# Kernel tuning notes

Hardware: AMD Instinct MI355X
Metric: run time of the kernel (lower is better)

Reference implementation:

```python
import jax, jax.numpy as jnp
import numpy as np
from jax.scipy.special import gammainc

ALPH = 0.8  # significance level (default arg in original forward)


def _median_width(X, iu, ju):
    # pairwise squared distances; original takes median of strictly-positive
    # strict-upper-triangle entries (tril subtracted) -> median over triu(k=1)
    G = jnp.sum(X * X, axis=1)                    # [n]
    D = G[:, None] + G[None, :] - 2.0 * (X @ X.T)  # [n, n]
    du = D[iu, ju]                                 # strict upper triangle, static size
    return jnp.sqrt(0.5 * jnp.median(du))


def _rbf(X, width):
    G = jnp.sum(X * X, axis=1)
    D = G[:, None] + G[None, :] - 2.0 * (X @ X.T)
    return jnp.exp(-D / (2.0 * width ** 2))


def _center(K):
    # H K H with H = I - 11^T/n  ==  K - rowmean - colmean + totalmean
    cm = jnp.mean(K, axis=0, keepdims=True)   # mean over rows  -> [1, n]
    rm = jnp.mean(K, axis=1, keepdims=True)   # mean over cols  -> [n, 1]
    tm = jnp.mean(K)
    return K - cm - rm + tm


def _gamma_ppf(a, p):
    # invert regularized lower incomplete gamma via fixed-iteration bisection
    hi0 = a + 10.0 * jnp.sqrt(a) + 100.0
    def body(i, lohi):
        lo, hi = lohi
        mid = 0.5 * (lo + hi)
        below = gammainc(a, mid) < p
        return (jnp.where(below, mid, lo), jnp.where(below, hi, mid))
    lo, hi = jax.lax.fori_loop(0, 100, body, (jnp.zeros_like(a), hi0))
    return 0.5 * (lo + hi)


def setup_inputs() -> dict:
    key = jax.random.key(0)
    k1, k2 = jax.random.split(key)
    X = jax.random.normal(k1, (4096, 64), dtype=jnp.float32)
    Y = jax.random.normal(k2, (4096, 64), dtype=jnp.float32)
    return {"X": X, "Y": Y}


def reference(X, Y):
    n = X.shape[0]
    iu, ju = np.triu_indices(n, k=1)  # static index set

    width_x = _median_width(X, iu, ju)
    width_y = _median_width(Y, iu, ju)

    K = _rbf(X, width_x)
    L = _rbf(Y, width_y)

    Kc = _center(K)
    Lc = _center(L)

    testStat = jnp.sum(Kc.T * Lc) / n

    V = (Kc * Lc / 6.0) ** 2
    varHSIC = (jnp.sum(V) - jnp.trace(V)) / n / (n - 1)
    varHSIC = varHSIC * 72.0 * (n - 4) * (n - 5) / n / (n - 1) / (n - 2) / (n - 3)

    # zero-diagonal kernels for mean estimate
    K0sum = jnp.sum(K) - jnp.trace(K)
    L0sum = jnp.sum(L) - jnp.trace(L)
    muX = K0sum / n / (n - 1)
    muY = L0sum / n / (n - 1)
    mHSIC = (1.0 + muX * muY - muX - muY) / n

    al = mHSIC ** 2 / varHSIC
    bet = varHSIC * n / mHSIC
    thresh = bet * _gamma_ppf(al, jnp.float32(1.0 - ALPH))
    return (testStat, thresh)
```

## Files before the change

kernel.cpp:

```cpp
#include <hip/hip_runtime.h>

typedef unsigned int u32;
typedef unsigned short u16;
typedef __attribute__((ext_vector_type(8))) short bf16x8;
typedef __attribute__((ext_vector_type(4))) float f32x4;

#define NPTS 4096
#define DIM  64
#define NB   32
#define NBLK 528
#define WLO16 0x4140u
#define NWBIN 832
#define RSTR 836
#define KF1C 8390654u
#define KF2C 8390656u


__device__ __forceinline__ void bmap(int b, int& by, int& bx){
  by = 0;
  while (b >= NB - by){ b -= NB - by; by++; }
  bx = by + b;
}

__device__ __forceinline__ u16 f2bf(float x){
  u32 u = __float_as_uint(x);
  return (u16)((u + 0x7fffu + ((u>>16)&1u)) >> 16);
}

__global__ __launch_bounds__(256) void convert_k(const float* __restrict__ X, const float* __restrict__ Y,
                                                 u16* __restrict__ Xbf, float* __restrict__ Gall,
                                                 u32* __restrict__ histsum, double* __restrict__ rowK,
                                                 double* __restrict__ rowL, double* __restrict__ sumsS,
                                                 double* __restrict__ slotbuf, u32* __restrict__ ctr){
  int t = blockIdx.x*256 + threadIdx.x;
  int rid = t >> 1, hf = t & 1;
  int z = rid >> 12, row = rid & 4095;
  const float* src = (z ? Y : X) + (size_t)row*DIM + hf*32;
  u16* basep = Xbf + ((size_t)z*32768 + (size_t)(row>>4)*128 + (row&15))*8;
  float g = 0.f;
#pragma unroll
  for (int f=0; f<4; f++){
    float4 f0 = *(const float4*)(src + f*8);
    float4 f1 = *(const float4*)(src + f*8 + 4);
    g = fmaf(f0.x,f0.x,g); g = fmaf(f0.y,f0.y,g); g = fmaf(f0.z,f0.z,g); g = fmaf(f0.w,f0.w,g);
    g = fmaf(f1.x,f1.x,g); g = fmaf(f1.y,f1.y,g); g = fmaf(f1.z,f1.z,g); g = fmaf(f1.w,f1.w,g);
    ushort4 h0, h1;
    h0.x=f2bf(f0.x); h0.y=f2bf(f0.y); h0.z=f2bf(f0.z); h0.w=f2bf(f0.w);
    h1.x=f2bf(f1.x); h1.y=f2bf(f1.y); h1.z=f2bf(f1.z); h1.w=f2bf(f1.w);
    u16* dst = basep + (size_t)(hf*4 + f)*16*8;
    *(ushort4*)dst = h0;
    *(ushort4*)(dst+4) = h1;
  }
  g += __shfl_xor(g, 1, 64);
  if (hf==0) Gall[rid] = g;
  if (t < NPTS){ rowK[t] = 0.0; rowL[t] = 0.0; }
  if (t < 2*RSTR) histsum[t] = 0u;
  if (t < 64) slotbuf[t] = 0.0;
  if (t < 16) sumsS[t] = 0.0;
  if (t == 0) *ctr = 0u;
}

__global__ __launch_bounds__(256,2) void hist_k(const u16* __restrict__ Xbf, const float* __restrict__ Gall,
                                                u32* __restrict__ histsum){
  __shared__ u32 lh[4][RSTR];
  int z = blockIdx.y, tid = threadIdx.x;
  int by,bx; bmap(blockIdx.x, by, bx);
  bool isdiag = (by==bx);
  u32 wgt = isdiag ? 1u : 2u;
  int w=tid>>6, lane=tid&63, q=lane>>4, nl=lane&15;
  int cp = lane & 3;
  for (int t=tid;t<4*RSTR;t+=256) ((u32*)lh)[t]=0;
  __syncthreads();
  const bf16x8* Xb = (const bf16x8*)Xbf + (size_t)z*32768;
  const float* Gz = Gall + z*NPTS;
  int ag0 = by*8 + w, ag1 = by*8 + 4 + w;
  bf16x8 a0f0 = Xb[ag0*128 + q*16 + nl];
  bf16x8 a0f1 = Xb[ag0*128 + (4+q)*16 + nl];
  bf16x8 a1f0 = Xb[ag1*128 + q*16 + nl];
  bf16x8 a1f1 = Xb[ag1*128 + (4+q)*16 + nl];
  float ga0 = Gz[ag0*16 + nl], ga1 = Gz[ag1*16 + nl];
  float g0m[4], g1m[4];
#pragma unroll
  for (int r=0;r<4;r++){ g0m[r] = __shfl(ga0, q*4+r, 64); g1m[r] = __shfl(ga1, q*4+r, 64); }
#pragma unroll
  for (int tb=0;tb<8;tb++){
    int jg = bx*8 + tb;
    bf16x8 bf0 = Xb[jg*128 + q*16 + nl];
    bf16x8 bf1 = Xb[jg*128 + (4+q)*16 + nl];
    f32x4 acc0 = (f32x4)0.0f, acc1 = (f32x4)0.0f;
    acc0 = __builtin_amdgcn_mfma_f32_16x16x32_bf16(a0f0, bf0, acc0, 0,0,0);
    acc0 = __builtin_amdgcn_mfma_f32_16x16x32_bf16(a0f1, bf1, acc0, 0,0,0);
    acc1 = __builtin_amdgcn_mfma_f32_16x16x32_bf16(a1f0, bf0, acc1, 0,0,0);
    acc1 = __builtin_amdgcn_mfma_f32_16x16x32_bf16(a1f1, bf1, acc1, 0,0,0);
    int j = jg*16 + nl;
    float gb = Gz[j];
#pragma unroll
    for (int r=0;r<4;r++){
      float d0 = (g0m[r] + gb) - 2.0f*acc0[r];
      float d1 = (g1m[r] + gb) - 2.0f*acc1[r];
      if (isdiag){
        if (ag0*16 + q*4 + r == j) d0 = 0.f;
        if (ag1*16 + q*4 + r == j) d1 = 0.f;
      }
      u32 t0 = __float_as_uint(d0) >> 16;
      u32 bin0 = (t0 < WLO16) ? 0u : (t0 >= WLO16+NWBIN) ? (u32)(NWBIN+1) : (t0 - WLO16 + 1u);
      atomicAdd(&lh[cp][bin0], wgt);
      u32 t1 = __float_as_uint(d1) >> 16;
      u32 bin1 = (t1 < WLO16) ? 0u : (t1 >= WLO16+NWBIN) ? (u32)(NWBIN+1) : (t1 - WLO16 + 1u);
      atomicAdd(&lh[cp][bin1], wgt);
    }
  }
  __syncthreads();
  u32* dst = histsum + (size_t)z*RSTR;
  for (int t=tid;t<RSTR;t+=256){
    u32 v = lh[0][t] + lh[1][t] + lh[2][t] + lh[3][t];
    if (v) atomicAdd(&dst[t], v);
  }
}

__global__ __launch_bounds__(256,2) void rowsum_k(const u16* __restrict__ Xbf, const float* __restrict__ Gall,
                                                  const u32* __restrict__ histsum, float* __restrict__ scal,
                                                  double* __restrict__ rowK, double* __restrict__ rowL,
                                                  double* __restrict__ sumsS){
  __shared__ union {
    struct { u32 wsum[4]; double svals[2]; float scal_sh; } sc;
    struct { double rowacc[128]; double colLDS[4][128]; double tred[2]; } rs;
  } sh;
  int z = blockIdx.y, tid = threadIdx.x;
  int w=tid>>6, lane=tid&63, q=lane>>4, nl=lane&15;

  {
    u32 c4[4] = {0,0,0,0};
    if (tid < 209){
      const u32* base = histsum + (size_t)z*RSTR + 4*tid;
      int lim = RSTR - 4*tid;
      c4[0] = base[0];
      if (lim>1) c4[1] = base[1];
      if (lim>2) c4[2] = base[2];
      if (lim>3) c4[3] = base[3];
    }
    u32 s = c4[0]+c4[1]+c4[2]+c4[3];
    u32 pre = s;
#pragma unroll
    for (int off=1; off<64; off<<=1){
      u32 t2 = __shfl_up(pre, off, 64);
      if (lane >= off) pre += t2;
    }
    if (lane==63) sh.sc.wsum[w] = pre;
    __syncthreads();
    u32 base2 = 0;
    for (int k=0;k<w;k++) base2 += sh.sc.wsum[k];
    u32 incl = base2 + pre, excl = incl - s;
    u32 ks[2] = {KF1C,KF2C};
#pragma unroll
    for (int w2=0; w2<2; w2++){
      if (ks[w2] >= excl && ks[w2] < incl){
        u32 acc = excl;
#pragma unroll
        for (int j=0;j<4;j++){
          if (ks[w2] < acc + c4[j]){
            int b = tid*4 + j;
            double lo, hi;
            if (b==0){ lo=12.0; hi=12.0; }
            else if (b>=NWBIN+1){ lo=1024.0; hi=1024.0; }
            else {
              u32 t16 = WLO16 + (u32)b - 1u;
              lo = (double)__uint_as_float(t16<<16);
              hi = (double)__uint_as_float((t16+1u)<<16);
            }
            double frac = ((double)(ks[w2]-acc) + 0.5)/(double)c4[j];
            sh.sc.svals[w2] = lo + (hi-lo)*frac;
            break;
          }
          acc += c4[j];
        }
      }
    }
    __syncthreads();
    if (tid==0){
      float med = (float)(0.5*(sh.sc.svals[0]+sh.sc.svals[1]));
      float wd = sqrtf(0.5f*med);
      float sc2 = 2.0f*wd*wd;
      sh.sc.scal_sh = sc2;
      if (blockIdx.x==0) scal[z] = sc2;
    }
    __syncthreads();
  }
  float negi = -1.0f / sh.sc.scal_sh;
  __syncthreads();

  int by,bx; bmap(blockIdx.x, by, bx);
  bool isdiag = (by==bx);
  const bf16x8* Xb = (const bf16x8*)Xbf + (size_t)z*32768;
  const float* Gz = Gall + z*NPTS;
  int ag0 = by*8 + w, ag1 = by*8 + 4 + w;
  bf16x8 a0f0 = Xb[ag0*128 + q*16 + nl];
  bf16x8 a0f1 = Xb[ag0*128 + (4+q)*16 + nl];
  bf16x8 a1f0 = Xb[ag1*128 + q*16 + nl];
  bf16x8 a1f1 = Xb[ag1*128 + (4+q)*16 + nl];
  float ga0 = Gz[ag0*16 + nl], ga1 = Gz[ag1*16 + nl];
  float g0m[4], g1m[4];
#pragma unroll
  for (int r=0;r<4;r++){ g0m[r] = __shfl(ga0, q*4+r, 64); g1m[r] = __shfl(ga1, q*4+r, 64); }
  double rs0[4] = {0,0,0,0}, rs1[4] = {0,0,0,0};
#pragma unroll
  for (int tb=0;tb<8;tb++){
    int jg = bx*8 + tb;
    bf16x8 bf0 = Xb[jg*128 + q*16 + nl];
    bf16x8 bf1 = Xb[jg*128 + (4+q)*16 + nl];
    f32x4 acc0 = (f32x4)0.0f, acc1 = (f32x4)0.0f;
    acc0 = __builtin_amdgcn_mfma_f32_16x16x32_bf16(a0f0, bf0, acc0, 0,0,0);
    acc0 = __builtin_amdgcn_mfma_f32_16x16x32_bf16(a0f1, bf1, acc0, 0,0,0);
    acc1 = __builtin_amdgcn_mfma_f32_16x16x32_bf16(a1f0, bf0, acc1, 0,0,0);
    acc1 = __builtin_amdgcn_mfma_f32_16x16x32_bf16(a1f1, bf1, acc1, 0,0,0);
    int j = jg*16 + nl;
    float gb = Gz[j];
    double cs = 0.0;
#pragma unroll
    for (int r=0;r<4;r++){
      float d0 = (g0m[r] + gb) - 2.0f*acc0[r];
      float d1 = (g1m[r] + gb) - 2.0f*acc1[r];
      if (isdiag){
        if (ag0*16 + q*4 + r == j) d0 = 0.f;
        if (ag1*16 + q*4 + r == j) d1 = 0.f;
      }
      double e0 = (double)expf(d0*negi);
      double e1 = (double)expf(d1*negi);
      rs0[r] += e0; rs1[r] += e1;
      cs += e0 + e1;
    }
    cs += __shfl_xor(cs, 16, 64);
    cs += __shfl_xor(cs, 32, 64);
    if (q==0) sh.rs.colLDS[w][tb*16 + nl] = cs;
  }
#pragma unroll
  for (int r=0;r<4;r++){
    double v0 = rs0[r], v1 = rs1[r];
    v0 += __shfl_xor(v0,1,64); v0 += __shfl_xor(v0,2,64);
    v0 += __shfl_xor(v0,4,64); v0 += __shfl_xor(v0,8,64);
    v1 += __shfl_xor(v1,1,64); v1 += __shfl_xor(v1,2,64);
    v1 += __shfl_xor(v1,4,64); v1 += __shfl_xor(v1,8,64);
    rs0[r] = v0; rs1[r] = v1;
  }
  if (nl==0){
#pragma unroll
    for (int r=0;r<4;r++){
      sh.rs.rowacc[w*16 + q*4 + r]     = rs0[r];
      sh.rs.rowacc[(4+w)*16 + q*4 + r] = rs1[r];
    }
  }
  __syncthreads();
  double tot = 0.0;
  if (tid < 128){
    double rv = sh.rs.rowacc[tid];
    double cv = sh.rs.colLDS[0][tid] + sh.rs.colLDS[1][tid] + sh.rs.colLDS[2][tid] + sh.rs.colLDS[3][tid];
    double* rowG = z ? rowL : rowK;
    atomicAdd(&rowG[by*128 + tid], rv);
    if (!isdiag) atomicAdd(&rowG[bx*128 + tid], cv);
    tot = rv + (isdiag ? 0.0 : cv);
  }
#pragma unroll
  for (int s2=1;s2<64;s2<<=1) tot += __shfl_xor(tot, s2, 64);
  if (lane==0 && w<2) sh.rs.tred[w] = tot;
  __syncthreads();
  if (tid==0) atomicAdd(&sumsS[z*8 + (blockIdx.x & 7)], sh.rs.tred[0] + sh.rs.tred[1]);
}

__device__ double gammainc_wave(double a, double x, double lga, int lane){
  double C = 1.0/a;
  double psum = 0.0;
  for (int b=0;b<8192;b++){
    double k = (double)(b*64 + lane + 1);
    double rr = x/(a+k);
    double pp = rr;
#pragma unroll
    for (int s=1;s<64;s<<=1){
      double t = __shfl_up(pp, s, 64);
      if (lane >= s) pp *= t;
    }
    double c = C*pp;
    psum += c;
    double clast = __shfl(c, 63, 64);
    double rlast = __shfl(rr, 63, 64);
    C = clast;
    if (rlast < 1.0 && clast*rlast/(1.0-rlast) < 1e-17) break;
  }
#pragma unroll
  for (int s=1;s<64;s<<=1) psum += __shfl_xor(psum, s, 64);
  double total = 1.0/a + psum;
  return exp(-x + a*log(x) - lga) * total;
}

__global__ __launch_bounds__(256,2) void final_k(const u16* __restrict__ Xbf, const float* __restrict__ Gall,
                                                 const float* __restrict__ scal,
                                                 const double* __restrict__ rowK,
                                                 const double* __restrict__ rowL,
                                                 const double* __restrict__ sumsS,
                                                 double* __restrict__ slotbuf, u32* __restrict__ ctr,
                                                 float* __restrict__ out){
  __shared__ double red[4][3];
  __shared__ int lastFlag;
  int tid = threadIdx.x;
  int b = blockIdx.x >> 1, half = blockIdx.x & 1;
  int by,bx; bmap(b,by,bx);
  bool isdiag = (by==bx);
  int w=tid>>6, lane=tid&63, q=lane>>4, nl=lane&15;
  const bf16x8* Xb = (const bf16x8*)Xbf;
  const bf16x8* Yb = Xb + 32768;
  const float* Gx = Gall;
  const float* Gy = Gall + NPTS;
  const double inv_n = 1.0/(double)NPTS;
  double sK=0.0, sL=0.0;
#pragma unroll
  for (int k2=0;k2<8;k2++){ sK += sumsS[k2]; sL += sumsS[8+k2]; }
  double tmK = sK*(inv_n*inv_n), tmL = sL*(inv_n*inv_n);
  float negx = -1.0f/scal[0], negy = -1.0f/scal[1];
  double wgt = isdiag ? 1.0 : 2.0;
  double S1=0, S2=0, trV=0;
  int ag = by*8 + half*4 + w;
  bf16x8 axf0 = Xb[ag*128 + q*16 + nl];
  bf16x8 axf1 = Xb[ag*128 + (4+q)*16 + nl];
  bf16x8 ayf0 = Yb[ag*128 + q*16 + nl];
  bf16x8 ayf1 = Yb[ag*128 + (4+q)*16 + nl];
  int rowA = ag*16 + nl;
  float gaX = Gx[rowA], gaY = Gy[rowA];
  float gXm[4], gYm[4];
#pragma unroll
  for (int r=0;r<4;r++){ gXm[r] = __shfl(gaX, q*4+r, 64); gYm[r] = __shfl(gaY, q*4+r, 64); }
  double rmKi[4], rmLi[4];
#pragma unroll
  for (int r=0;r<4;r++){
    int i = ag*16 + q*4 + r;
    rmKi[r] = rowK[i]*inv_n; rmLi[r] = rowL[i]*inv_n;
  }
#pragma unroll
  for (int tb=0;tb<8;tb++){
    int jg = bx*8 + tb;
    f32x4 accX = (f32x4)0.0f, accY = (f32x4)0.0f;
    accX = __builtin_amdgcn_mfma_f32_16x16x32_bf16(axf0, Xb[jg*128 + q*16 + nl],     accX, 0,0,0);
    accX = __builtin_amdgcn_mfma_f32_16x16x32_bf16(axf1, Xb[jg*128 + (4+q)*16 + nl], accX, 0,0,0);
    accY = __builtin_amdgcn_mfma_f32_16x16x32_bf16(ayf0, Yb[jg*128 + q*16 + nl],     accY, 0,0,0);
    accY = __builtin_amdgcn_mfma_f32_16x16x32_bf16(ayf1, Yb[jg*128 + (4+q)*16 + nl], accY, 0,0,0);
    int j = jg*16 + nl;
    float gbX = Gx[j], gbY = Gy[j];
    double cmK = rowK[j]*inv_n - tmK;
    double cmL = rowL[j]*inv_n - tmL;
#pragma unroll
    for (int r=0;r<4;r++){
      int i = ag*16 + q*4 + r;
      float dx = (gXm[r] + gbX) - 2.0f*accX[r];
      float dy = (gYm[r] + gbY) - 2.0f*accY[r];
      bool dg = isdiag && i==j;
      if (dg){ dx = 0.f; dy = 0.f; }
      float kx = expf(dx*negx);
      float lv = expf(dy*negy);
      double kc = ((double)kx - rmKi[r]) - cmK;
      double lc = ((double)lv - rmLi[r]) - cmL;
      double prod = kc*lc;
      S1 += wgt*prod;
      double vv = (prod*prod)*(1.0/36.0);
      S2 += wgt*vv;
      if (dg) trV += vv;
    }
  }
  double vals[3]={S1,S2,trV};
#pragma unroll
  for (int v=0;v<3;v++){
    double x = vals[v];
#pragma unroll
    for (int s2=1;s2<64;s2<<=1) x += __shfl_xor(x, s2, 64);
    if (lane==0) red[w][v]=x;
  }
  __syncthreads();
  if (tid < 3){
    double val = red[0][tid]+red[1][tid]+red[2][tid]+red[3][tid];
    atomicAdd(&slotbuf[(size_t)(blockIdx.x & 15)*4 + tid], val);
  }
  __syncthreads();
  if (tid==0){
    __threadfence();
    u32 old = atomicAdd(ctr, 1u);
    lastFlag = (old == (u32)(2*NBLK - 1)) ? 1 : 0;
  }
  __syncthreads();
  if (!lastFlag) return;

  if (tid >= 64) return;
  double t0=0.0, t1=0.0, t2=0.0;
  if (lane < 16){
    double* sp = slotbuf + (size_t)lane*4;
    t0 = atomicAdd(&sp[0], 0.0);
    t1 = atomicAdd(&sp[1], 0.0);
    t2 = atomicAdd(&sp[2], 0.0);
  }
#pragma unroll
  for (int s2=1;s2<64;s2<<=1){
    t0 += __shfl_xor(t0, s2, 64);
    t1 += __shfl_xor(t1, s2, 64);
    t2 += __shfl_xor(t2, s2, 64);
  }
  const double n = (double)NPTS;
  double S1t=t0, S2t=t1, trVt=t2;
  double testStat = S1t/n;
  double varHSIC = (S2t - trVt)/n/(n-1.0);
  varHSIC = varHSIC*72.0*(n-4.0)*(n-5.0)/n/(n-1.0)/(n-2.0)/(n-3.0);
  double muX = (sK-n)/n/(n-1.0);
  double muY = (sL-n)/n/(n-1.0);
  double mHSIC = (1.0 + muX*muY - muX - muY)/n;
  double al = mHSIC*mHSIC/varHSIC;
  double bet = varHSIC*n/mHSIC;
  double p = (double)((float)(1.0-0.8));
  double lga = lgamma(al);
  double lo = 0.0, hi = al + 10.0*sqrt(al) + 100.0;
  const double zp = -0.8416212335729142957;
  double tt = 1.0 - 1.0/(9.0*al) + zp/(3.0*sqrt(al));
  double x = al*tt*tt*tt;
  if (!(x > 0.0) || !(x < hi)) x = 0.5*hi;
  for (int it=0; it<2; ++it){
    double P = gammainc_wave(al, x, lga, lane);
    double diff = P - p;
    if (diff < 0.0) lo = x; else hi = x;
    if (fabs(diff) < 1e-12) break;
    double pdf = exp(-x + (al-1.0)*log(x) - lga);
    double nx = x - diff/pdf;
    if (!(nx > lo) || !(nx < hi)) nx = 0.5*(lo+hi);
    x = nx;
  }
  if (lane==0){
    out[0]=(float)testStat;
    out[1]=(float)(bet*x);
  }
}

extern "C" void kernel_launch(void* const* d_in, const int* in_sizes, int n_in,
                              void* d_out, int out_size, void* d_ws, size_t ws_size,
                              hipStream_t stream) {
  const float* X = (const float*)d_in[0];
  const float* Y = (const float*)d_in[1];
  float* out = (float*)d_out;
  char* ws = (char*)d_ws;

  double* sumsS    = (double*)ws;
  float*  scal     = (float*)(ws + 128);
  u32*    histsum  = (u32*)(ws + 256);
  double* slotbuf  = (double*)(ws + 7168);
  u32*    ctr      = (u32*)(ws + 7680);
  double* rowK     = (double*)(ws + 8192);
  double* rowL     = (double*)(ws + 40960);
  float*  Gall     = (float*)(ws + 73728);
  u16*    Xbf      = (u16*)(ws + (4u<<20));
  size_t need = (size_t)(4u<<20) + (size_t)2*NPTS*DIM*2;

  if (ws_size < need) return;

  convert_k<<<64,256,0,stream>>>(X, Y, Xbf, Gall, histsum, rowK, rowL, sumsS, slotbuf, ctr);
  hist_k<<<dim3(NBLK,2),256,0,stream>>>(Xbf, Gall, histsum);
  rowsum_k<<<dim3(NBLK,2),256,0,stream>>>(Xbf, Gall, histsum, scal, rowK, rowL, sumsS);
  final_k<<<2*NBLK,256,0,stream>>>(Xbf, Gall, scal, rowK, rowL, sumsS, slotbuf, ctr, out);
}
```

Baseline: 153.6 us.

## Stage B tiles in LDS, merge final_k halves, block-parallel gammainc series

In all three pairwise kernels, the 128-column B tile is staged once into shared memory instead of each wave reading it from global memory. final_k now has each block cover both row halves, halving the grid and sharing each B-fragment load across two A sets. The gammainc series in the last block is spread across all four waves with a cross-wave prefix product, which adds two barriers per iteration. The threadfence before the completion counter is dropped and replaced by consuming the atomic's return value, which is a memory-ordering risk.

```diff
diff --git a/kernel.cpp b/kernel.cpp
--- a/kernel.cpp
+++ b/kernel.cpp
@@ -63,15 +63,18 @@
 __global__ __launch_bounds__(256,2) void hist_k(const u16* __restrict__ Xbf, const float* __restrict__ Gall,
                                                 u32* __restrict__ histsum){
   __shared__ u32 lh[4][RSTR];
+  __shared__ bf16x8 sB[1024];
   int z = blockIdx.y, tid = threadIdx.x;
   int by,bx; bmap(blockIdx.x, by, bx);
   bool isdiag = (by==bx);
   u32 wgt = isdiag ? 1u : 2u;
   int w=tid>>6, lane=tid&63, q=lane>>4, nl=lane&15;
   int cp = lane & 3;
+  const bf16x8* Xb = (const bf16x8*)Xbf + (size_t)z*32768;
+  const bf16x8* srcB = Xb + (size_t)(bx*8)*128;
+  for (int t=tid;t<1024;t+=256) sB[t] = srcB[t];
   for (int t=tid;t<4*RSTR;t+=256) ((u32*)lh)[t]=0;
   __syncthreads();
-  const bf16x8* Xb = (const bf16x8*)Xbf + (size_t)z*32768;
   const float* Gz = Gall + z*NPTS;
   int ag0 = by*8 + w, ag1 = by*8 + 4 + w;
   bf16x8 a0f0 = Xb[ag0*128 + q*16 + nl];
@@ -84,15 +87,14 @@
   for (int r=0;r<4;r++){ g0m[r] = __shfl(ga0, q*4+r, 64); g1m[r] = __shfl(ga1, q*4+r, 64); }
 #pragma unroll
   for (int tb=0;tb<8;tb++){
-    int jg = bx*8 + tb;
-    bf16x8 bf0 = Xb[jg*128 + q*16 + nl];
-    bf16x8 bf1 = Xb[jg*128 + (4+q)*16 + nl];
+    bf16x8 bf0 = sB[tb*128 + q*16 + nl];
+    bf16x8 bf1 = sB[tb*128 + (4+q)*16 + nl];
     f32x4 acc0 = (f32x4)0.0f, acc1 = (f32x4)0.0f;
     acc0 = __builtin_amdgcn_mfma_f32_16x16x32_bf16(a0f0, bf0, acc0, 0,0,0);
     acc0 = __builtin_amdgcn_mfma_f32_16x16x32_bf16(a0f1, bf1, acc0, 0,0,0);
     acc1 = __builtin_amdgcn_mfma_f32_16x16x32_bf16(a1f0, bf0, acc1, 0,0,0);
     acc1 = __builtin_amdgcn_mfma_f32_16x16x32_bf16(a1f1, bf1, acc1, 0,0,0);
-    int j = jg*16 + nl;
+    int j = (bx*8 + tb)*16 + nl;
     float gb = Gz[j];
 #pragma unroll
     for (int r=0;r<4;r++){
@@ -126,8 +128,14 @@
     struct { u32 wsum[4]; double svals[2]; float scal_sh; } sc;
     struct { double rowacc[128]; double colLDS[4][128]; double tred[2]; } rs;
   } sh;
+  __shared__ bf16x8 sB[1024];
   int z = blockIdx.y, tid = threadIdx.x;
   int w=tid>>6, lane=tid&63, q=lane>>4, nl=lane&15;
+  int by,bx; bmap(blockIdx.x, by, bx);
+  bool isdiag = (by==bx);
+  const bf16x8* Xb = (const bf16x8*)Xbf + (size_t)z*32768;
+  const bf16x8* srcB = Xb + (size_t)(bx*8)*128;
+  for (int t=tid;t<1024;t+=256) sB[t] = srcB[t];
 
   {
     u32 c4[4] = {0,0,0,0};
@@ -189,9 +197,6 @@
   float negi = -1.0f / sh.sc.scal_sh;
   __syncthreads();
 
-  int by,bx; bmap(blockIdx.x, by, bx);
-  bool isdiag = (by==bx);
-  const bf16x8* Xb = (const bf16x8*)Xbf + (size_t)z*32768;
   const float* Gz = Gall + z*NPTS;
   int ag0 = by*8 + w, ag1 = by*8 + 4 + w;
   bf16x8 a0f0 = Xb[ag0*128 + q*16 + nl];
@@ -205,15 +210,14 @@
   double rs0[4] = {0,0,0,0}, rs1[4] = {0,0,0,0};
 #pragma unroll
   for (int tb=0;tb<8;tb++){
-    int jg = bx*8 + tb;
-    bf16x8 bf0 = Xb[jg*128 + q*16 + nl];
-    bf16x8 bf1 = Xb[jg*128 + (4+q)*16 + nl];
+    bf16x8 bf0 = sB[tb*128 + q*16 + nl];
+    bf16x8 bf1 = sB[tb*128 + (4+q)*16 + nl];
     f32x4 acc0 = (f32x4)0.0f, acc1 = (f32x4)0.0f;
     acc0 = __builtin_amdgcn_mfma_f32_16x16x32_bf16(a0f0, bf0, acc0, 0,0,0);
     acc0 = __builtin_amdgcn_mfma_f32_16x16x32_bf16(a0f1, bf1, acc0, 0,0,0);
     acc1 = __builtin_amdgcn_mfma_f32_16x16x32_bf16(a1f0, bf0, acc1, 0,0,0);
     acc1 = __builtin_amdgcn_mfma_f32_16x16x32_bf16(a1f1, bf1, acc1, 0,0,0);
-    int j = jg*16 + nl;
+    int j = (bx*8 + tb)*16 + nl;
     float gb = Gz[j];
     double cs = 0.0;
 #pragma unroll
@@ -266,11 +270,13 @@
   if (tid==0) atomicAdd(&sumsS[z*8 + (blockIdx.x & 7)], sh.rs.tred[0] + sh.rs.tred[1]);
 }
 
-__device__ double gammainc_wave(double a, double x, double lga, int lane){
+__device__ double gammainc_block(double a, double x, double lga,
+                                 int tid, int lane, int w,
+                                 double* wp , double* bs ){
   double C = 1.0/a;
   double psum = 0.0;
-  for (int b=0;b<8192;b++){
-    double k = (double)(b*64 + lane + 1);
+  for (int b=0;b<2048;b++){
+    double k = (double)(b*256 + tid + 1);
     double rr = x/(a+k);
     double pp = rr;
 #pragma unroll
@@ -278,16 +284,26 @@
       double t = __shfl_up(pp, s, 64);
       if (lane >= s) pp *= t;
     }
-    double c = C*pp;
+    double wtot = __shfl(pp, 63, 64);
+    if (lane==0) wp[w] = wtot;
+    __syncthreads();
+    double cross = 1.0;
+    for (int k2=0;k2<w;k2++) cross *= wp[k2];
+    double call = wp[0]*wp[1]*wp[2]*wp[3];
+    double c = C*cross*pp;
     psum += c;
-    double clast = __shfl(c, 63, 64);
-    double rlast = __shfl(rr, 63, 64);
-    C = clast;
-    if (rlast < 1.0 && clast*rlast/(1.0-rlast) < 1e-17) break;
+    double Cn = C*call;
+    C = Cn;
+    double rlast = x/(a + (double)(b*256 + 256));
+    __syncthreads();
+    if (rlast < 1.0 && Cn*rlast/(1.0-rlast) < 1e-17) break;
   }
 #pragma unroll
   for (int s=1;s<64;s<<=1) psum += __shfl_xor(psum, s, 64);
-  double total = 1.0/a + psum;
+  if (lane==0) bs[w] = psum;
+  __syncthreads();
+  double total = 1.0/a + bs[0]+bs[1]+bs[2]+bs[3];
+  __syncthreads();
   return exp(-x + a*log(x) - lga) * total;
 }
 
@@ -298,15 +314,20 @@
                                                  const double* __restrict__ sumsS,
                                                  double* __restrict__ slotbuf, u32* __restrict__ ctr,
                                                  float* __restrict__ out){
+  __shared__ bf16x8 sBX[1024];
+  __shared__ bf16x8 sBY[1024];
   __shared__ double red[4][3];
+  __shared__ double gwp[4], gbs[4], stot[3];
   __shared__ int lastFlag;
   int tid = threadIdx.x;
-  int b = blockIdx.x >> 1, half = blockIdx.x & 1;
-  int by,bx; bmap(b,by,bx);
+  int by,bx; bmap(blockIdx.x,by,bx);
   bool isdiag = (by==bx);
   int w=tid>>6, lane=tid&63, q=lane>>4, nl=lane&15;
   const bf16x8* Xb = (const bf16x8*)Xbf;
   const bf16x8* Yb = Xb + 32768;
+  const bf16x8* srcBX = Xb + (size_t)(bx*8)*128;
+  const bf16x8* srcBY = Yb + (size_t)(bx*8)*128;
+  for (int t=tid;t<1024;t+=256){ sBX[t] = srcBX[t]; sBY[t] = srcBY[t]; }
   const float* Gx = Gall;
   const float* Gy = Gall + NPTS;
   const double inv_n = 1.0/(double)NPTS;
@@ -317,50 +338,82 @@
   float negx = -1.0f/scal[0], negy = -1.0f/scal[1];
   double wgt = isdiag ? 1.0 : 2.0;
   double S1=0, S2=0, trV=0;
-  int ag = by*8 + half*4 + w;
-  bf16x8 axf0 = Xb[ag*128 + q*16 + nl];
-  bf16x8 axf1 = Xb[ag*128 + (4+q)*16 + nl];
-  bf16x8 ayf0 = Yb[ag*128 + q*16 + nl];
-  bf16x8 ayf1 = Yb[ag*128 + (4+q)*16 + nl];
-  int rowA = ag*16 + nl;
-  float gaX = Gx[rowA], gaY = Gy[rowA];
-  float gXm[4], gYm[4];
-#pragma unroll
-  for (int r=0;r<4;r++){ gXm[r] = __shfl(gaX, q*4+r, 64); gYm[r] = __shfl(gaY, q*4+r, 64); }
-  double rmKi[4], rmLi[4];
+  int agA = by*8 + w;
+  int agB = by*8 + 4 + w;
+  bf16x8 axf0A = Xb[agA*128 + q*16 + nl];
+  bf16x8 axf1A = Xb[agA*128 + (4+q)*16 + nl];
+  bf16x8 ayf0A = Yb[agA*128 + q*16 + nl];
+  bf16x8 ayf1A = Yb[agA*128 + (4+q)*16 + nl];
+  bf16x8 axf0B = Xb[agB*128 + q*16 + nl];
+  bf16x8 axf1B = Xb[agB*128 + (4+q)*16 + nl];
+  bf16x8 ayf0B = Yb[agB*128 + q*16 + nl];
+  bf16x8 ayf1B = Yb[agB*128 + (4+q)*16 + nl];
+  float gaXA = Gx[agA*16 + nl], gaYA = Gy[agA*16 + nl];
+  float gaXB = Gx[agB*16 + nl], gaYB = Gy[agB*16 + nl];
+  float gXmA[4], gYmA[4], gXmB[4], gYmB[4];
 #pragma unroll
   for (int r=0;r<4;r++){
-    int i = ag*16 + q*4 + r;
-    rmKi[r] = rowK[i]*inv_n; rmLi[r] = rowL[i]*inv_n;
-  }
+    gXmA[r] = __shfl(gaXA, q*4+r, 64); gYmA[r] = __shfl(gaYA, q*4+r, 64);
+    gXmB[r] = __shfl(gaXB, q*4+r, 64); gYmB[r] = __shfl(gaYB, q*4+r, 64);
+  }
+  double rmKiA[4], rmLiA[4], rmKiB[4], rmLiB[4];
+#pragma unroll
+  for (int r=0;r<4;r++){
+    int iA = agA*16 + q*4 + r, iB = agB*16 + q*4 + r;
+    rmKiA[r] = rowK[iA]*inv_n; rmLiA[r] = rowL[iA]*inv_n;
+    rmKiB[r] = rowK[iB]*inv_n; rmLiB[r] = rowL[iB]*inv_n;
+  }
+  __syncthreads();
 #pragma unroll
   for (int tb=0;tb<8;tb++){
-    int jg = bx*8 + tb;
-    f32x4 accX = (f32x4)0.0f, accY = (f32x4)0.0f;
-    accX = __builtin_amdgcn_mfma_f32_16x16x32_bf16(axf0, Xb[jg*128 + q*16 + nl],     accX, 0,0,0);
-    accX = __builtin_amdgcn_mfma_f32_16x16x32_bf16(axf1, Xb[jg*128 + (4+q)*16 + nl], accX, 0,0,0);
-    accY = __builtin_amdgcn_mfma_f32_16x16x32_bf16(ayf0, Yb[jg*128 + q*16 + nl],     accY, 0,0,0);
-    accY = __builtin_amdgcn_mfma_f32_16x16x32_bf16(ayf1, Yb[jg*128 + (4+q)*16 + nl], accY, 0,0,0);
-    int j = jg*16 + nl;
+    bf16x8 bx0 = sBX[tb*128 + q*16 + nl];
+    bf16x8 bx1 = sBX[tb*128 + (4+q)*16 + nl];
+    bf16x8 by0 = sBY[tb*128 + q*16 + nl];
+    bf16x8 by1 = sBY[tb*128 + (4+q)*16 + nl];
+    f32x4 aXA = (f32x4)0.0f, aYA = (f32x4)0.0f, aXB = (f32x4)0.0f, aYB = (f32x4)0.0f;
+    aXA = __builtin_amdgcn_mfma_f32_16x16x32_bf16(axf0A, bx0, aXA, 0,0,0);
+    aXA = __builtin_amdgcn_mfma_f32_16x16x32_bf16(axf1A, bx1, aXA, 0,0,0);
+    aYA = __builtin_amdgcn_mfma_f32_16x16x32_bf16(ayf0A, by0, aYA, 0,0,0);
+    aYA = __builtin_amdgcn_mfma_f32_16x16x32_bf16(ayf1A, by1, aYA, 0,0,0);
+    aXB = __builtin_amdgcn_mfma_f32_16x16x32_bf16(axf0B, bx0, aXB, 0,0,0);
+    aXB = __builtin_amdgcn_mfma_f32_16x16x32_bf16(axf1B, bx1, aXB, 0,0,0);
+    aYB = __builtin_amdgcn_mfma_f32_16x16x32_bf16(ayf0B, by0, aYB, 0,0,0);
+    aYB = __builtin_amdgcn_mfma_f32_16x16x32_bf16(ayf1B, by1, aYB, 0,0,0);
+    int j = (bx*8 + tb)*16 + nl;
     float gbX = Gx[j], gbY = Gy[j];
     double cmK = rowK[j]*inv_n - tmK;
     double cmL = rowL[j]*inv_n - tmL;
 #pragma unroll
     for (int r=0;r<4;r++){
-      int i = ag*16 + q*4 + r;
-      float dx = (gXm[r] + gbX) - 2.0f*accX[r];
-      float dy = (gYm[r] + gbY) - 2.0f*accY[r];
-      bool dg = isdiag && i==j;
-      if (dg){ dx = 0.f; dy = 0.f; }
-      float kx = expf(dx*negx);
-      float lv = expf(dy*negy);
-      double kc = ((double)kx - rmKi[r]) - cmK;
-      double lc = ((double)lv - rmLi[r]) - cmL;
-      double prod = kc*lc;
-      S1 += wgt*prod;
-      double vv = (prod*prod)*(1.0/36.0);
-      S2 += wgt*vv;
-      if (dg) trV += vv;
+      int iA = agA*16 + q*4 + r;
+      float dxA = (gXmA[r] + gbX) - 2.0f*aXA[r];
+      float dyA = (gYmA[r] + gbY) - 2.0f*aYA[r];
+      bool dgA = isdiag && iA==j;
+      if (dgA){ dxA = 0.f; dyA = 0.f; }
+      float kxA = expf(dxA*negx);
+      float lvA = expf(dyA*negy);
+      double kcA = ((double)kxA - rmKiA[r]) - cmK;
+      double lcA = ((double)lvA - rmLiA[r]) - cmL;
+      double prodA = kcA*lcA;
+      S1 += wgt*prodA;
+      double vvA = (prodA*prodA)*(1.0/36.0);
+      S2 += wgt*vvA;
+      if (dgA) trV += vvA;
+
+      int iB = agB*16 + q*4 + r;
+      float dxB = (gXmB[r] + gbX) - 2.0f*aXB[r];
+      float dyB = (gYmB[r] + gbY) - 2.0f*aYB[r];
+      bool dgB = isdiag && iB==j;
+      if (dgB){ dxB = 0.f; dyB = 0.f; }
+      float kxB = expf(dxB*negx);
+      float lvB = expf(dyB*negy);
+      double kcB = ((double)kxB - rmKiB[r]) - cmK;
+      double lcB = ((double)lvB - rmLiB[r]) - cmL;
+      double prodB = kcB*lcB;
+      S1 += wgt*prodB;
+      double vvB = (prodB*prodB)*(1.0/36.0);
+      S2 += wgt*vvB;
+      if (dgB) trV += vvB;
     }
   }
   double vals[3]={S1,S2,trV};
@@ -374,33 +427,36 @@
   __syncthreads();
   if (tid < 3){
     double val = red[0][tid]+red[1][tid]+red[2][tid]+red[3][tid];
-    atomicAdd(&slotbuf[(size_t)(blockIdx.x & 15)*4 + tid], val);
+    double old = atomicAdd(&slotbuf[(size_t)(blockIdx.x & 15)*4 + tid], val);
+    asm volatile("" :: "v"(old));
   }
   __syncthreads();
   if (tid==0){
-    __threadfence();
     u32 old = atomicAdd(ctr, 1u);
-    lastFlag = (old == (u32)(2*NBLK - 1)) ? 1 : 0;
+    lastFlag = (old == (u32)(NBLK - 1)) ? 1 : 0;
   }
   __syncthreads();
   if (!lastFlag) return;
 
-  if (tid >= 64) return;
-  double t0=0.0, t1=0.0, t2=0.0;
-  if (lane < 16){
-    double* sp = slotbuf + (size_t)lane*4;
-    t0 = atomicAdd(&sp[0], 0.0);
-    t1 = atomicAdd(&sp[1], 0.0);
-    t2 = atomicAdd(&sp[2], 0.0);
-  }
-#pragma unroll
-  for (int s2=1;s2<64;s2<<=1){
-    t0 += __shfl_xor(t0, s2, 64);
-    t1 += __shfl_xor(t1, s2, 64);
-    t2 += __shfl_xor(t2, s2, 64);
-  }
+  if (w==0){
+    double t0=0.0, t1=0.0, t2=0.0;
+    if (lane < 16){
+      double* sp = slotbuf + (size_t)lane*4;
+      t0 = atomicAdd(&sp[0], 0.0);
+      t1 = atomicAdd(&sp[1], 0.0);
+      t2 = atomicAdd(&sp[2], 0.0);
+    }
+#pragma unroll
+    for (int s2=1;s2<16;s2<<=1){
+      t0 += __shfl_xor(t0, s2, 64);
+      t1 += __shfl_xor(t1, s2, 64);
+      t2 += __shfl_xor(t2, s2, 64);
+    }
+    if (lane==0){ stot[0]=t0; stot[1]=t1; stot[2]=t2; }
+  }
+  __syncthreads();
   const double n = (double)NPTS;
-  double S1t=t0, S2t=t1, trVt=t2;
+  double S1t=stot[0], S2t=stot[1], trVt=stot[2];
   double testStat = S1t/n;
   double varHSIC = (S2t - trVt)/n/(n-1.0);
   varHSIC = varHSIC*72.0*(n-4.0)*(n-5.0)/n/(n-1.0)/(n-2.0)/(n-3.0);
@@ -417,7 +473,7 @@
   double x = al*tt*tt*tt;
   if (!(x > 0.0) || !(x < hi)) x = 0.5*hi;
   for (int it=0; it<2; ++it){
-    double P = gammainc_wave(al, x, lga, lane);
+    double P = gammainc_block(al, x, lga, tid, lane, w, gwp, gbs);
     double diff = P - p;
     if (diff < 0.0) lo = x; else hi = x;
     if (fabs(diff) < 1e-12) break;
@@ -426,7 +482,7 @@
     if (!(nx > lo) || !(nx < hi)) nx = 0.5*(lo+hi);
     x = nx;
   }
-  if (lane==0){
+  if (tid==0){
     out[0]=(float)testStat;
     out[1]=(float)(bet*x);
   }
@@ -456,5 +512,5 @@
   convert_k<<<64,256,0,stream>>>(X, Y, Xbf, Gall, histsum, rowK, rowL, sumsS, slotbuf, ctr);
   hist_k<<<dim3(NBLK,2),256,0,stream>>>(Xbf, Gall, histsum);
   rowsum_k<<<dim3(NBLK,2),256,0,stream>>>(Xbf, Gall, histsum, scal, rowK, rowL, sumsS);
-  final_k<<<2*NBLK,256,0,stream>>>(Xbf, Gall, scal, rowK, rowL, sumsS, slotbuf, ctr, out);
-}
+  final_k<<<NBLK,256,0,stream>>>(Xbf, Gall, scal, rowK, rowL, sumsS, slotbuf, ctr, out);
+}
```

Result: faster. 145.5 us (-5.3%).

## Stage B tiles in LDS, use exp2f, raise occupancy, parallelize gammainc across block

Applied to the files above, without the earlier changes.

Each of hist_k, rowsum_k and final_k now copies the block's B-column tile into shared memory once and reads the MFMA operands from there instead of global memory. Occupancy hints go from 2 to 4 blocks per CU, and expf becomes exp2f with log2(e) folded into the scale. final_k applies the weights once outside the inner loop, computes the series term with an FMA, and drops a threadfence. The incomplete-gamma series in the last block now spreads four terms per thread over all 256 threads instead of one wave. The trade-offs are more LDS use, extra barriers, and a possible register-pressure limit at the higher occupancy.

```diff
diff --git a/kernel.cpp b/kernel.cpp
--- a/kernel.cpp
+++ b/kernel.cpp
@@ -12,6 +12,7 @@
 #define WLO16 0x4140u
 #define NWBIN 832
 #define RSTR 836
+#define LOG2E 1.4426950408889634f
 #define KF1C 8390654u
 #define KF2C 8390656u
 
@@ -60,18 +61,21 @@
   if (t == 0) *ctr = 0u;
 }
 
-__global__ __launch_bounds__(256,2) void hist_k(const u16* __restrict__ Xbf, const float* __restrict__ Gall,
+__global__ __launch_bounds__(256,4) void hist_k(const u16* __restrict__ Xbf, const float* __restrict__ Gall,
                                                 u32* __restrict__ histsum){
   __shared__ u32 lh[4][RSTR];
+  __shared__ bf16x8 sB[1024];
   int z = blockIdx.y, tid = threadIdx.x;
   int by,bx; bmap(blockIdx.x, by, bx);
   bool isdiag = (by==bx);
   u32 wgt = isdiag ? 1u : 2u;
   int w=tid>>6, lane=tid&63, q=lane>>4, nl=lane&15;
   int cp = lane & 3;
+  const bf16x8* Xb = (const bf16x8*)Xbf + (size_t)z*32768;
+  const bf16x8* srcB = Xb + (size_t)(bx*8)*128;
+  for (int t=tid;t<1024;t+=256) sB[t] = srcB[t];
   for (int t=tid;t<4*RSTR;t+=256) ((u32*)lh)[t]=0;
   __syncthreads();
-  const bf16x8* Xb = (const bf16x8*)Xbf + (size_t)z*32768;
   const float* Gz = Gall + z*NPTS;
   int ag0 = by*8 + w, ag1 = by*8 + 4 + w;
   bf16x8 a0f0 = Xb[ag0*128 + q*16 + nl];
@@ -84,15 +88,14 @@
   for (int r=0;r<4;r++){ g0m[r] = __shfl(ga0, q*4+r, 64); g1m[r] = __shfl(ga1, q*4+r, 64); }
 #pragma unroll
   for (int tb=0;tb<8;tb++){
-    int jg = bx*8 + tb;
-    bf16x8 bf0 = Xb[jg*128 + q*16 + nl];
-    bf16x8 bf1 = Xb[jg*128 + (4+q)*16 + nl];
+    bf16x8 bf0 = sB[tb*128 + q*16 + nl];
+    bf16x8 bf1 = sB[tb*128 + (4+q)*16 + nl];
     f32x4 acc0 = (f32x4)0.0f, acc1 = (f32x4)0.0f;
     acc0 = __builtin_amdgcn_mfma_f32_16x16x32_bf16(a0f0, bf0, acc0, 0,0,0);
     acc0 = __builtin_amdgcn_mfma_f32_16x16x32_bf16(a0f1, bf1, acc0, 0,0,0);
     acc1 = __builtin_amdgcn_mfma_f32_16x16x32_bf16(a1f0, bf0, acc1, 0,0,0);
     acc1 = __builtin_amdgcn_mfma_f32_16x16x32_bf16(a1f1, bf1, acc1, 0,0,0);
-    int j = jg*16 + nl;
+    int j = (bx*8 + tb)*16 + nl;
     float gb = Gz[j];
 #pragma unroll
     for (int r=0;r<4;r++){
@@ -118,7 +121,7 @@
   }
 }
 
-__global__ __launch_bounds__(256,2) void rowsum_k(const u16* __restrict__ Xbf, const float* __restrict__ Gall,
+__global__ __launch_bounds__(256,4) void rowsum_k(const u16* __restrict__ Xbf, const float* __restrict__ Gall,
                                                   const u32* __restrict__ histsum, float* __restrict__ scal,
                                                   double* __restrict__ rowK, double* __restrict__ rowL,
                                                   double* __restrict__ sumsS){
@@ -126,8 +129,14 @@
     struct { u32 wsum[4]; double svals[2]; float scal_sh; } sc;
     struct { double rowacc[128]; double colLDS[4][128]; double tred[2]; } rs;
   } sh;
+  __shared__ bf16x8 sB[1024];
   int z = blockIdx.y, tid = threadIdx.x;
   int w=tid>>6, lane=tid&63, q=lane>>4, nl=lane&15;
+  int by,bx; bmap(blockIdx.x, by, bx);
+  bool isdiag = (by==bx);
+  const bf16x8* Xb = (const bf16x8*)Xbf + (size_t)z*32768;
+  const bf16x8* srcB = Xb + (size_t)(bx*8)*128;
+  for (int t=tid;t<1024;t+=256) sB[t] = srcB[t];
 
   {
     u32 c4[4] = {0,0,0,0};
@@ -186,12 +195,9 @@
     }
     __syncthreads();
   }
-  float negi = -1.0f / sh.sc.scal_sh;
-  __syncthreads();
-
-  int by,bx; bmap(blockIdx.x, by, bx);
-  bool isdiag = (by==bx);
-  const bf16x8* Xb = (const bf16x8*)Xbf + (size_t)z*32768;
+  float negi = -LOG2E / sh.sc.scal_sh;
+  __syncthreads();
+
   const float* Gz = Gall + z*NPTS;
   int ag0 = by*8 + w, ag1 = by*8 + 4 + w;
   bf16x8 a0f0 = Xb[ag0*128 + q*16 + nl];
@@ -205,15 +211,14 @@
   double rs0[4] = {0,0,0,0}, rs1[4] = {0,0,0,0};
 #pragma unroll
   for (int tb=0;tb<8;tb++){
-    int jg = bx*8 + tb;
-    bf16x8 bf0 = Xb[jg*128 + q*16 + nl];
-    bf16x8 bf1 = Xb[jg*128 + (4+q)*16 + nl];
+    bf16x8 bf0 = sB[tb*128 + q*16 + nl];
+    bf16x8 bf1 = sB[tb*128 + (4+q)*16 + nl];
     f32x4 acc0 = (f32x4)0.0f, acc1 = (f32x4)0.0f;
     acc0 = __builtin_amdgcn_mfma_f32_16x16x32_bf16(a0f0, bf0, acc0, 0,0,0);
     acc0 = __builtin_amdgcn_mfma_f32_16x16x32_bf16(a0f1, bf1, acc0, 0,0,0);
     acc1 = __builtin_amdgcn_mfma_f32_16x16x32_bf16(a1f0, bf0, acc1, 0,0,0);
     acc1 = __builtin_amdgcn_mfma_f32_16x16x32_bf16(a1f1, bf1, acc1, 0,0,0);
-    int j = jg*16 + nl;
+    int j = (bx*8 + tb)*16 + nl;
     float gb = Gz[j];
     double cs = 0.0;
 #pragma unroll
@@ -224,8 +229,8 @@
         if (ag0*16 + q*4 + r == j) d0 = 0.f;
         if (ag1*16 + q*4 + r == j) d1 = 0.f;
       }
-      double e0 = (double)expf(d0*negi);
-      double e1 = (double)expf(d1*negi);
+      double e0 = (double)exp2f(d0*negi);
+      double e1 = (double)exp2f(d1*negi);
       rs0[r] += e0; rs1[r] += e1;
       cs += e0 + e1;
     }
@@ -266,39 +271,58 @@
   if (tid==0) atomicAdd(&sumsS[z*8 + (blockIdx.x & 7)], sh.rs.tred[0] + sh.rs.tred[1]);
 }
 
-__device__ double gammainc_wave(double a, double x, double lga, int lane){
+__device__ double gammainc_block4(double a, double x, double lga,
+                                  int tid, int lane, int w,
+                                  double* wp , double* bs ){
   double C = 1.0/a;
   double psum = 0.0;
-  for (int b=0;b<8192;b++){
-    double k = (double)(b*64 + lane + 1);
-    double rr = x/(a+k);
-    double pp = rr;
+  for (int b=0;b<512;b++){
+    double k0 = (double)(b*1024 + tid*4);
+    double r1 = x/(a+k0+1.0), r2 = x/(a+k0+2.0), r3 = x/(a+k0+3.0), r4 = x/(a+k0+4.0);
+    double p12 = r1*r2;
+    double pl = p12*(r3*r4);
+    double pp = pl;
 #pragma unroll
     for (int s=1;s<64;s<<=1){
       double t = __shfl_up(pp, s, 64);
       if (lane >= s) pp *= t;
     }
-    double c = C*pp;
-    psum += c;
-    double clast = __shfl(c, 63, 64);
-    double rlast = __shfl(rr, 63, 64);
-    C = clast;
-    if (rlast < 1.0 && clast*rlast/(1.0-rlast) < 1e-17) break;
+    if (lane==63) wp[w] = pp;
+    __syncthreads();
+    double cross = 1.0;
+    for (int k2=0;k2<w;k2++) cross *= wp[k2];
+    double call = wp[0]*wp[1]*wp[2]*wp[3];
+    double excl = __shfl_up(pp, 1, 64);
+    if (lane==0) excl = 1.0;
+    double base = C*cross*excl;
+    double t1 = base*r1, t2 = base*p12, t3 = t2*r3, t4 = base*pl;
+    psum += (t1+t2)+(t3+t4);
+    double Cn = C*call;
+    C = Cn;
+    double rlast = x/(a + (double)(b*1024 + 1024));
+    __syncthreads();
+    if (rlast < 1.0 && Cn*rlast/(1.0-rlast) < 1e-17) break;
   }
 #pragma unroll
   for (int s=1;s<64;s<<=1) psum += __shfl_xor(psum, s, 64);
-  double total = 1.0/a + psum;
+  if (lane==0) bs[w] = psum;
+  __syncthreads();
+  double total = 1.0/a + bs[0]+bs[1]+bs[2]+bs[3];
+  __syncthreads();
   return exp(-x + a*log(x) - lga) * total;
 }
 
-__global__ __launch_bounds__(256,2) void final_k(const u16* __restrict__ Xbf, const float* __restrict__ Gall,
+__global__ __launch_bounds__(256,4) void final_k(const u16* __restrict__ Xbf, const float* __restrict__ Gall,
                                                  const float* __restrict__ scal,
                                                  const double* __restrict__ rowK,
                                                  const double* __restrict__ rowL,
                                                  const double* __restrict__ sumsS,
                                                  double* __restrict__ slotbuf, u32* __restrict__ ctr,
                                                  float* __restrict__ out){
+  __shared__ bf16x8 sBX[1024];
+  __shared__ bf16x8 sBY[1024];
   __shared__ double red[4][3];
+  __shared__ double gwp[4], gbs[4], stot[3];
   __shared__ int lastFlag;
   int tid = threadIdx.x;
   int b = blockIdx.x >> 1, half = blockIdx.x & 1;
@@ -307,6 +331,9 @@
   int w=tid>>6, lane=tid&63, q=lane>>4, nl=lane&15;
   const bf16x8* Xb = (const bf16x8*)Xbf;
   const bf16x8* Yb = Xb + 32768;
+  const bf16x8* srcBX = Xb + (size_t)(bx*8)*128;
+  const bf16x8* srcBY = Yb + (size_t)(bx*8)*128;
+  for (int t=tid;t<1024;t+=256){ sBX[t] = srcBX[t]; sBY[t] = srcBY[t]; }
   const float* Gx = Gall;
   const float* Gy = Gall + NPTS;
   const double inv_n = 1.0/(double)NPTS;
@@ -314,16 +341,14 @@
 #pragma unroll
   for (int k2=0;k2<8;k2++){ sK += sumsS[k2]; sL += sumsS[8+k2]; }
   double tmK = sK*(inv_n*inv_n), tmL = sL*(inv_n*inv_n);
-  float negx = -1.0f/scal[0], negy = -1.0f/scal[1];
-  double wgt = isdiag ? 1.0 : 2.0;
+  float negx = -LOG2E/scal[0], negy = -LOG2E/scal[1];
   double S1=0, S2=0, trV=0;
   int ag = by*8 + half*4 + w;
   bf16x8 axf0 = Xb[ag*128 + q*16 + nl];
   bf16x8 axf1 = Xb[ag*128 + (4+q)*16 + nl];
   bf16x8 ayf0 = Yb[ag*128 + q*16 + nl];
   bf16x8 ayf1 = Yb[ag*128 + (4+q)*16 + nl];
-  int rowA = ag*16 + nl;
-  float gaX = Gx[rowA], gaY = Gy[rowA];
+  float gaX = Gx[ag*16 + nl], gaY = Gy[ag*16 + nl];
   float gXm[4], gYm[4];
 #pragma unroll
   for (int r=0;r<4;r++){ gXm[r] = __shfl(gaX, q*4+r, 64); gYm[r] = __shfl(gaY, q*4+r, 64); }
@@ -333,15 +358,19 @@
     int i = ag*16 + q*4 + r;
     rmKi[r] = rowK[i]*inv_n; rmLi[r] = rowL[i]*inv_n;
   }
+  __syncthreads();
 #pragma unroll
   for (int tb=0;tb<8;tb++){
-    int jg = bx*8 + tb;
+    bf16x8 bx0 = sBX[tb*128 + q*16 + nl];
+    bf16x8 bx1 = sBX[tb*128 + (4+q)*16 + nl];
+    bf16x8 by0 = sBY[tb*128 + q*16 + nl];
+    bf16x8 by1 = sBY[tb*128 + (4+q)*16 + nl];
     f32x4 accX = (f32x4)0.0f, accY = (f32x4)0.0f;
-    accX = __builtin_amdgcn_mfma_f32_16x16x32_bf16(axf0, Xb[jg*128 + q*16 + nl],     accX, 0,0,0);
-    accX = __builtin_amdgcn_mfma_f32_16x16x32_bf16(axf1, Xb[jg*128 + (4+q)*16 + nl], accX, 0,0,0);
-    accY = __builtin_amdgcn_mfma_f32_16x16x32_bf16(ayf0, Yb[jg*128 + q*16 + nl],     accY, 0,0,0);
-    accY = __builtin_amdgcn_mfma_f32_16x16x32_bf16(ayf1, Yb[jg*128 + (4+q)*16 + nl], accY, 0,0,0);
-    int j = jg*16 + nl;
+    accX = __builtin_amdgcn_mfma_f32_16x16x32_bf16(axf0, bx0, accX, 0,0,0);
+    accX = __builtin_amdgcn_mfma_f32_16x16x32_bf16(axf1, bx1, accX, 0,0,0);
+    accY = __builtin_amdgcn_mfma_f32_16x16x32_bf16(ayf0, by0, accY, 0,0,0);
+    accY = __builtin_amdgcn_mfma_f32_16x16x32_bf16(ayf1, by1, accY, 0,0,0);
+    int j = (bx*8 + tb)*16 + nl;
     float gbX = Gx[j], gbY = Gy[j];
     double cmK = rowK[j]*inv_n - tmK;
     double cmL = rowL[j]*inv_n - tmL;
@@ -352,16 +381,21 @@
       float dy = (gYm[r] + gbY) - 2.0f*accY[r];
       bool dg = isdiag && i==j;
       if (dg){ dx = 0.f; dy = 0.f; }
-      float kx = expf(dx*negx);
-      float lv = expf(dy*negy);
+      float kx = exp2f(dx*negx);
+      float lv = exp2f(dy*negy);
       double kc = ((double)kx - rmKi[r]) - cmK;
       double lc = ((double)lv - rmLi[r]) - cmL;
       double prod = kc*lc;
-      S1 += wgt*prod;
-      double vv = (prod*prod)*(1.0/36.0);
-      S2 += wgt*vv;
-      if (dg) trV += vv;
-    }
+      S1 += prod;
+      S2 = fma(prod, prod, S2);
+      if (dg) trV = fma(prod, prod, trV);
+    }
+  }
+  {
+    double wgt = isdiag ? 1.0 : 2.0;
+    S1 *= wgt;
+    S2 *= wgt*(1.0/36.0);
+    trV *= (1.0/36.0);
   }
   double vals[3]={S1,S2,trV};
 #pragma unroll
@@ -374,33 +408,36 @@
   __syncthreads();
   if (tid < 3){
     double val = red[0][tid]+red[1][tid]+red[2][tid]+red[3][tid];
-    atomicAdd(&slotbuf[(size_t)(blockIdx.x & 15)*4 + tid], val);
+    double old = atomicAdd(&slotbuf[(size_t)(blockIdx.x & 15)*4 + tid], val);
+    asm volatile("" :: "v"(old));
   }
   __syncthreads();
   if (tid==0){
-    __threadfence();
     u32 old = atomicAdd(ctr, 1u);
     lastFlag = (old == (u32)(2*NBLK - 1)) ? 1 : 0;
   }
   __syncthreads();
   if (!lastFlag) return;
 
-  if (tid >= 64) return;
-  double t0=0.0, t1=0.0, t2=0.0;
-  if (lane < 16){
-    double* sp = slotbuf + (size_t)lane*4;
-    t0 = atomicAdd(&sp[0], 0.0);
-    t1 = atomicAdd(&sp[1], 0.0);
-    t2 = atomicAdd(&sp[2], 0.0);
-  }
-#pragma unroll
-  for (int s2=1;s2<64;s2<<=1){
-    t0 += __shfl_xor(t0, s2, 64);
-    t1 += __shfl_xor(t1, s2, 64);
-    t2 += __shfl_xor(t2, s2, 64);
-  }
+  if (w==0){
+    double t0=0.0, t1=0.0, t2=0.0;
+    if (lane < 16){
+      double* sp = slotbuf + (size_t)lane*4;
+      t0 = atomicAdd(&sp[0], 0.0);
+      t1 = atomicAdd(&sp[1], 0.0);
+      t2 = atomicAdd(&sp[2], 0.0);
+    }
+#pragma unroll
+    for (int s2=1;s2<16;s2<<=1){
+      t0 += __shfl_xor(t0, s2, 64);
+      t1 += __shfl_xor(t1, s2, 64);
+      t2 += __shfl_xor(t2, s2, 64);
+    }
+    if (lane==0){ stot[0]=t0; stot[1]=t1; stot[2]=t2; }
+  }
+  __syncthreads();
   const double n = (double)NPTS;
-  double S1t=t0, S2t=t1, trVt=t2;
+  double S1t=stot[0], S2t=stot[1], trVt=stot[2];
   double testStat = S1t/n;
   double varHSIC = (S2t - trVt)/n/(n-1.0);
   varHSIC = varHSIC*72.0*(n-4.0)*(n-5.0)/n/(n-1.0)/(n-2.0)/(n-3.0);
@@ -417,7 +454,7 @@
   double x = al*tt*tt*tt;
   if (!(x > 0.0) || !(x < hi)) x = 0.5*hi;
   for (int it=0; it<2; ++it){
-    double P = gammainc_wave(al, x, lga, lane);
+    double P = gammainc_block4(al, x, lga, tid, lane, w, gwp, gbs);
     double diff = P - p;
     if (diff < 0.0) lo = x; else hi = x;
     if (fabs(diff) < 1e-12) break;
@@ -426,7 +463,7 @@
     if (!(nx > lo) || !(nx < hi)) nx = 0.5*(lo+hi);
     x = nx;
   }
-  if (lane==0){
+  if (tid==0){
     out[0]=(float)testStat;
     out[1]=(float)(bet*x);
   }
```

Result: faster. 144.6 us (-5.9%).
